# Optimization experiments

Hardware: AMD Instinct MI355X
Metric: run time of the kernel (lower is better)

Reference implementation:

```python
import jax, jax.numpy as jnp
import numpy as np

D_MODEL = 1024
N_HEADS = 16
HEAD_DIM = D_MODEL // N_HEADS
RSQRT = 1.0 / np.sqrt(HEAD_DIM).astype(np.float32)


def setup_inputs() -> dict:
    key = jax.random.key(0)
    k1, k2, k3 = jax.random.split(key, 3)
    bs, sl = 4, 2048
    x = jax.random.normal(k1, (bs, sl, D_MODEL), dtype=jnp.float32)
    # stored as (in, out) so forward is x @ w; same math as torch Linear (no bias)
    w_qkv = jax.random.normal(k2, (D_MODEL, 3 * D_MODEL), dtype=jnp.float32) * 0.02
    w_proj = jax.random.normal(k3, (D_MODEL, D_MODEL), dtype=jnp.float32) * 0.02
    return {"x": x, "w_qkv": w_qkv, "w_proj": w_proj}


def reference(x, w_qkv, w_proj):
    bs, sl, dm = x.shape
    qkv = x @ w_qkv                                   # (bs, sl, 3*dm)
    q, k, v = jnp.split(qkv, 3, axis=-1)
    # (bs, sl, n, hd) -> (bs, n, sl, hd)
    q = q.reshape(bs, sl, N_HEADS, HEAD_DIM).transpose(0, 2, 1, 3)
    k = k.reshape(bs, sl, N_HEADS, HEAD_DIM).transpose(0, 2, 1, 3)
    v = v.reshape(bs, sl, N_HEADS, HEAD_DIM).transpose(0, 2, 1, 3)
    attn = jnp.einsum("bnqd,bnkd->bnqk", q, k) * RSQRT  # (bs, n, sl, sl)
    causal = jnp.tril(jnp.ones((sl, sl), dtype=bool))
    attn = jnp.where(causal[None, None], attn, -jnp.inf)
    attn = jax.nn.softmax(attn, axis=-1)
    out = jnp.einsum("bnqk,bnkd->bnqd", attn, v)      # (bs, n, sl, hd)
    out = out.transpose(0, 2, 1, 3).reshape(bs, sl, dm)
    return out @ w_proj
```

## Files before the change

kernel.cpp:

```cpp
#include <hip/hip_runtime.h>
#include <stdint.h>
#include <math.h>

typedef __attribute__((ext_vector_type(8))) short short8;
typedef __attribute__((ext_vector_type(4))) float f32x4;
typedef __attribute__((ext_vector_type(16))) float f32x16;

#define DEV __device__ __forceinline__

DEV unsigned short f2bf(float f) {
  union { float f; unsigned int u; } v; v.f = f;
  return (unsigned short)((v.u + 0x7FFFu + ((v.u >> 16) & 1u)) >> 16);
}

DEV unsigned int pkbf(float a, float b) {
  unsigned int r;
  asm("v_cvt_pk_bf16_f32 %0, %1, %2" : "=v"(r) : "v"(a), "v"(b));
  return r;
}

#if __has_builtin(__builtin_amdgcn_permlane32_swap)
DEV float redsum32(float v) {
  typedef __attribute__((ext_vector_type(2))) unsigned int uint2v;
  union { float f; unsigned int u; } c; c.f = v;
  uint2v r = __builtin_amdgcn_permlane32_swap(c.u, c.u, false, false);
  union { unsigned int u; float f; } a, b; a.u = r[0]; b.u = r[1];
  return a.f + b.f;
}
#else
DEV float redsum32(float v) { return v + __shfl_xor(v, 32, 64); }
#endif

DEV void gld16(const void* g, void* lds) {
  __builtin_amdgcn_global_load_lds(
      (const __attribute__((address_space(1))) unsigned int*)g,
      (__attribute__((address_space(3))) unsigned int*)lds, 16, 0, 0);
}

__global__ __launch_bounds__(256) void cvt_bf16_kernel(
    const float* __restrict__ in, unsigned short* __restrict__ out, int n) {
  int i = (blockIdx.x * 256 + threadIdx.x) * 8;
  if (i >= n) return;
  const float4 a = *(const float4*)(in + i);
  const float4 b = *(const float4*)(in + i + 4);
  short8 o;
  o[0] = (short)f2bf(a.x); o[1] = (short)f2bf(a.y);
  o[2] = (short)f2bf(a.z); o[3] = (short)f2bf(a.w);
  o[4] = (short)f2bf(b.x); o[5] = (short)f2bf(b.y);
  o[6] = (short)f2bf(b.z); o[7] = (short)f2bf(b.w);
  *(short8*)(out + i) = o;
}

__global__ __launch_bounds__(256) void transpose_w_kernel(
    const float* __restrict__ in, unsigned short* __restrict__ out,
    int Kdim, int Ndim) {
  __shared__ float t[32][33];
  const int nb = blockIdx.x * 32, kb = blockIdx.y * 32;
  const int tx = threadIdx.x & 31, ty = threadIdx.x >> 5;
#pragma unroll
  for (int i = 0; i < 32; i += 8)
    t[ty + i][tx] = in[(size_t)(kb + ty + i) * Ndim + nb + tx];
  __syncthreads();
#pragma unroll
  for (int i = 0; i < 32; i += 8)
    out[(size_t)(nb + ty + i) * Kdim + kb + tx] = f2bf(t[tx][ty + i]);
}

template<int M, int N, int K, int MODE>
__global__ __launch_bounds__(256)
void gemm_bt_kernel(const unsigned short* __restrict__ A,
                    const unsigned short* __restrict__ Bt,
                    unsigned short* __restrict__ Qd,
                    unsigned short* __restrict__ Kd,
                    unsigned short* __restrict__ Vd,
                    float* __restrict__ outC) {
  __shared__ __align__(16) unsigned short lsA[128 * 32];
  __shared__ __align__(16) unsigned short lsB[128 * 32];
  const int tid = threadIdx.x, wid = tid >> 6, lane = tid & 63;
  const int wr = wid >> 1, wc = wid & 1;
  constexpr int nx = N / 128;
  constexpr int nwg = (M / 128) * nx;
  static_assert(nwg % 8 == 0, "bijective XCD swizzle needs nwg % 8 == 0");
  int id = blockIdx.y * nx + blockIdx.x;
  id = (id & 7) * (nwg / 8) + (id >> 3);
  const int m0 = (id / nx) * 128, n0 = (id % nx) * 128;

  f32x4 acc[4][4] = {};

  const int rA = lane >> 2, kA = (lane & 3) * 8;
  for (int kt = 0; kt < K / 32; ++kt) {
    __syncthreads();
#pragma unroll
    for (int c = 0; c < 2; ++c) {
      const int q = c * 4 + wid;
      gld16(A  + (size_t)(m0 + q * 16 + rA) * K + kt * 32 + kA, lsA + q * 512);
      gld16(Bt + (size_t)(n0 + q * 16 + rA) * K + kt * 32 + kA, lsB + q * 512);
    }
    __syncthreads();
    short8 af[4], bfr[4];
#pragma unroll
    for (int i = 0; i < 4; ++i) {
      af[i]  = *(const short8*)(lsA + (wr * 64 + i * 16 + (lane & 15)) * 32 + (lane >> 4) * 8);
      bfr[i] = *(const short8*)(lsB + (wc * 64 + i * 16 + (lane & 15)) * 32 + (lane >> 4) * 8);
    }
#pragma unroll
    for (int i = 0; i < 4; ++i)
#pragma unroll
      for (int j = 0; j < 4; ++j)
        acc[i][j] = __builtin_amdgcn_mfma_f32_16x16x32_bf16(af[i], bfr[j], acc[i][j], 0, 0, 0);
  }

#pragma unroll
  for (int i = 0; i < 4; ++i) {
#pragma unroll
    for (int j = 0; j < 4; ++j) {
      const int rbase = m0 + wr * 64 + i * 16 + (lane >> 4) * 4;
      const int col = n0 + wc * 64 + j * 16 + (lane & 15);
      if constexpr (MODE == 0) {
        const int which = col >> 10, hh = (col >> 6) & 15, d = col & 63;
        unsigned short* dst = which == 0 ? Qd : (which == 1 ? Kd : Vd);
        const float scale = which == 0 ? 0.18033688f : 1.0f;
        const int sd = d >> 4, hi = (d >> 3) & 1, jd = d & 7;
        const int t2 = d >> 5, qlv = d & 31;
#pragma unroll
        for (int ii = 0; ii < 4; ++ii) {
          const int r = rbase + ii, b = r >> 11, seq = r & 2047;
          size_t idx;
          if (which == 2) {
            const int kt2 = seq >> 5, sl = (seq >> 4) & 1, g = seq & 15;
            const int u = (g & 3) | ((g & 4) << 1) | ((g & 8) >> 1);
            idx = ((((size_t)(b * 16 + hh) * 64 + kt2) * 4 + (t2 * 2 + sl)) * 64
                   + qlv + 32 * (u >> 3)) * 8 + (u & 7);
          } else {
            idx = ((((size_t)(b * 16 + hh) * 64 + (seq >> 5)) * 4 + sd) * 64
                   + (seq & 31) + 32 * hi) * 8 + jd;
          }
          dst[idx] = f2bf(acc[i][j][ii] * scale);
        }
      } else {
#pragma unroll
        for (int ii = 0; ii < 4; ++ii)
          outC[(size_t)(rbase + ii) * N + col] = acc[i][j][ii];
      }
    }
  }
}

DEV void loadK4f(const unsigned short* Kfb, int kt, int lane, short8 kf[4]) {
  const unsigned short* p = Kfb + (size_t)kt * 2048 + lane * 8;
#pragma unroll
  for (int s = 0; s < 4; ++s) kf[s] = *(const short8*)(p + s * 512);
}
DEV void loadV4f(const unsigned short* Vfb, int kt, int lane, short8 vf[4]) {
  const unsigned short* p = Vfb + (size_t)kt * 2048 + lane * 8;
#pragma unroll
  for (int f = 0; f < 4; ++f) vf[f] = *(const short8*)(p + f * 512);
}

template<int NP, bool MASK>
DEV void attn_step(int kv0, const short8 kf[4], const short8 qf[][4],
                   const int q0[], const short8 vf[4],
                   float l[], f32x16 o[][2], int ql, int h) {
  f32x16 st[NP];
  __builtin_amdgcn_s_setprio(1);
#pragma unroll
  for (int pp = 0; pp < NP; ++pp) {
    f32x16 s = {};
#pragma unroll
    for (int ss = 0; ss < 4; ++ss)
      s = __builtin_amdgcn_mfma_f32_32x32x16_bf16(kf[ss], qf[pp][ss], s, 0, 0, 0);
    st[pp] = s;
  }
  __builtin_amdgcn_s_setprio(0);
  if constexpr (MASK) {
#pragma unroll
    for (int r = 0; r < 16; ++r) {
      const int krow = (r & 3) + 8 * (r >> 2) + 4 * h;
      if (kv0 + krow > q0[0] + ql) st[0][r] = -INFINITY;
    }
  }
  union pk_t { unsigned int u[4]; short8 s8; };
  pk_t f0[NP], f1[NP];
#pragma unroll
  for (int pp = 0; pp < NP; ++pp) {
    float p[16];
#pragma unroll
    for (int r = 0; r < 16; ++r) p[r] = exp2f(fminf(st[pp][r], 64.f));
    float ps = ((p[0] + p[1]) + (p[2] + p[3])) + ((p[4] + p[5]) + (p[6] + p[7]));
    ps += ((p[8] + p[9]) + (p[10] + p[11])) + ((p[12] + p[13]) + (p[14] + p[15]));
    l[pp] += ps;
#pragma unroll
    for (int i = 0; i < 4; ++i) {
      f0[pp].u[i] = pkbf(p[2 * i], p[2 * i + 1]);
      f1[pp].u[i] = pkbf(p[8 + 2 * i], p[9 + 2 * i]);
    }
  }
  __builtin_amdgcn_s_setprio(1);
#pragma unroll
  for (int pp = 0; pp < NP; ++pp) {
    o[pp][0] = __builtin_amdgcn_mfma_f32_32x32x16_bf16(vf[0], f0[pp].s8, o[pp][0], 0, 0, 0);
    o[pp][0] = __builtin_amdgcn_mfma_f32_32x32x16_bf16(vf[1], f1[pp].s8, o[pp][0], 0, 0, 0);
    o[pp][1] = __builtin_amdgcn_mfma_f32_32x32x16_bf16(vf[2], f0[pp].s8, o[pp][1], 0, 0, 0);
    o[pp][1] = __builtin_amdgcn_mfma_f32_32x32x16_bf16(vf[3], f1[pp].s8, o[pp][1], 0, 0, 0);
  }
  __builtin_amdgcn_s_setprio(0);
}

__global__ __launch_bounds__(256, 2)
void attn_kernel(const unsigned short* __restrict__ Qf,
                 const unsigned short* __restrict__ Kf,
                 const unsigned short* __restrict__ Vf,
                 unsigned short* __restrict__ O) {
  const int bh = blockIdx.x & 63;
  const int w  = blockIdx.x >> 6;
  const int wid = threadIdx.x >> 6, lane = threadIdx.x & 63;
  const int ql = lane & 31, h = lane >> 5;
  const int qtA = w * 4 + wid;
  const int qtB = 63 - qtA;
  const int q0[2] = {qtA * 32, qtB * 32};

  const unsigned short* Qfb = Qf + (size_t)bh * 131072;
  const unsigned short* Kfb = Kf + (size_t)bh * 131072;
  const unsigned short* Vfb = Vf + (size_t)bh * 131072;

  short8 qf[2][4];
#pragma unroll
  for (int pp = 0; pp < 2; ++pp) {
    const int qt = pp == 0 ? qtA : qtB;
#pragma unroll
    for (int s = 0; s < 4; ++s)
      qf[pp][s] = *(const short8*)(Qfb + (size_t)qt * 2048 + s * 512 + lane * 8);
  }

  f32x16 o[2][2] = {};
  float l[2] = {0.f, 0.f};

  short8 kf[4], kn[4], vf[4];
  loadK4f(Kfb, 0, lane, kf);

  for (int t = 0; t < qtA; ++t) {
    loadV4f(Vfb, t, lane, vf);
    loadK4f(Kfb, t + 1, lane, kn);
    attn_step<2, false>(0, kf, qf, q0, vf, l, o, ql, h);
#pragma unroll
    for (int s = 0; s < 4; ++s) kf[s] = kn[s];
  }
  {
    loadV4f(Vfb, qtA, lane, vf);
    loadK4f(Kfb, qtA + 1, lane, kn);
    attn_step<2, true>(qtA * 32, kf, qf, q0, vf, l, o, ql, h);
#pragma unroll
    for (int s = 0; s < 4; ++s) kf[s] = kn[s];
  }
  for (int t = qtA + 1; t < qtB; ++t) {
    loadV4f(Vfb, t, lane, vf);
    loadK4f(Kfb, t + 1, lane, kn);
    attn_step<1, false>(0, kf, &qf[1], &q0[1], vf, &l[1], &o[1], ql, h);
#pragma unroll
    for (int s = 0; s < 4; ++s) kf[s] = kn[s];
  }
  {
    loadV4f(Vfb, qtB, lane, vf);
    attn_step<1, true>(qtB * 32, kf, &qf[1], &q0[1], vf, &l[1], &o[1], ql, h);
  }

  const int b = bh >> 4, head = bh & 15;
#pragma unroll
  for (int pp = 0; pp < 2; ++pp) {
    const float inv = 1.0f / redsum32(l[pp]);
    unsigned short* Orow = O + ((size_t)(b * 2048 + q0[pp] + ql)) * 1024 + head * 64;
#pragma unroll
    for (int g = 0; g < 4; ++g) {
      {
        const unsigned int lo = pkbf(o[pp][0][g * 4 + 0] * inv, o[pp][0][g * 4 + 1] * inv);
        const unsigned int hi = pkbf(o[pp][0][g * 4 + 2] * inv, o[pp][0][g * 4 + 3] * inv);
        uint2 val; val.x = lo; val.y = hi;
        *(uint2*)(Orow + 8 * g + 4 * h) = val;
      }
      {
        const unsigned int lo = pkbf(o[pp][1][g * 4 + 0] * inv, o[pp][1][g * 4 + 1] * inv);
        const unsigned int hi = pkbf(o[pp][1][g * 4 + 2] * inv, o[pp][1][g * 4 + 3] * inv);
        uint2 val; val.x = lo; val.y = hi;
        *(uint2*)(Orow + 32 + 8 * g + 4 * h) = val;
      }
    }
  }
}

extern "C" void kernel_launch(void* const* d_in, const int* in_sizes, int n_in,
                              void* d_out, int out_size, void* d_ws, size_t ws_size,
                              hipStream_t stream) {
  (void)in_sizes; (void)n_in; (void)out_size; (void)ws_size;
  const float* x      = (const float*)d_in[0];
  const float* w_qkv  = (const float*)d_in[1];
  const float* w_proj = (const float*)d_in[2];
  float* out = (float*)d_out;
  char* ws = (char*)d_ws;

  unsigned short* x_bf   = (unsigned short*)(ws);
  unsigned short* wqT    = (unsigned short*)(ws + 16777216);
  unsigned short* wpT    = (unsigned short*)(ws + 23068672);
  unsigned short* Qfd    = (unsigned short*)(ws + 25165824);
  unsigned short* Kfd    = (unsigned short*)(ws + 41943040);
  unsigned short* Vfd    = (unsigned short*)(ws + 58720256);
  unsigned short* attn_o = x_bf;

  cvt_bf16_kernel<<<4096, 256, 0, stream>>>(x, x_bf, 8388608);
  transpose_w_kernel<<<dim3(96, 32), 256, 0, stream>>>(w_qkv, wqT, 1024, 3072);
  transpose_w_kernel<<<dim3(32, 32), 256, 0, stream>>>(w_proj, wpT, 1024, 1024);
  gemm_bt_kernel<8192, 3072, 1024, 0><<<dim3(24, 64), 256, 0, stream>>>(
      x_bf, wqT, Qfd, Kfd, Vfd, nullptr);
  attn_kernel<<<512, 256, 0, stream>>>(Qfd, Kfd, Vfd, attn_o);
  gemm_bt_kernel<8192, 1024, 1024, 1><<<dim3(8, 64), 256, 0, stream>>>(
      attn_o, wpT, nullptr, nullptr, nullptr, out);
}
```

Before: 183.5 us.

## Split attention KV range across two waves per query tile and combine via LDS

Doubles the attention block to 512 threads so each query-tile pair is handled by two waves that take alternating (even/odd) key tiles, then merges their partial outputs and row sums through shared memory before normalizing and writing. The aim is more wave-level parallelism and latency hiding in the attention kernel, which had only 4 waves per block with long serial KV loops. The merge relies on softmax without running-max rescaling, so the two partials can simply be added. In exchange it adds an LDS combine, a block barrier, and a larger LDS footprint, and the prefetch stride of two tiles may weaken cache reuse.

```diff
diff --git a/kernel.cpp b/kernel.cpp
--- a/kernel.cpp
+++ b/kernel.cpp
@@ -206,18 +206,28 @@
   __builtin_amdgcn_s_setprio(0);
 }
 
-__global__ __launch_bounds__(256, 2)
+__global__ __launch_bounds__(512)
 void attn_kernel(const unsigned short* __restrict__ Qf,
                  const unsigned short* __restrict__ Kf,
                  const unsigned short* __restrict__ Vf,
                  unsigned short* __restrict__ O) {
+  __shared__ __align__(16) f32x4 cmb[4][16][64];
+  __shared__ float cml[4][2][64];
   const int bh = blockIdx.x & 63;
   const int w  = blockIdx.x >> 6;
   const int wid = threadIdx.x >> 6, lane = threadIdx.x & 63;
+  const int widp = wid & 3, piv = wid >> 2;
   const int ql = lane & 31, h = lane >> 5;
-  const int qtA = w * 4 + wid;
+  const int qtA = w * 4 + widp;
   const int qtB = 63 - qtA;
   const int q0[2] = {qtA * 32, qtB * 32};
+
+  const int L = qtA - ((qtA - piv) & 1);
+  const bool ownA = ((qtA & 1) == piv);
+  const int stopU = ownA ? qtA - 2 : L;
+  const int sB = L + 2;
+  const bool ownB = !ownA;
+  const int stopB = ownB ? qtB - 2 : qtB - 1;
 
   const unsigned short* Qfb = Qf + (size_t)bh * 131072;
   const unsigned short* Kfb = Kf + (size_t)bh * 131072;
@@ -236,52 +246,80 @@
   float l[2] = {0.f, 0.f};
 
   short8 kf[4], kn[4], vf[4];
-  loadK4f(Kfb, 0, lane, kf);
-
-  for (int t = 0; t < qtA; ++t) {
+  loadK4f(Kfb, piv, lane, kf);
+
+  for (int t = piv; t <= stopU; t += 2) {
     loadV4f(Vfb, t, lane, vf);
-    loadK4f(Kfb, t + 1, lane, kn);
+    loadK4f(Kfb, t + 2, lane, kn);
     attn_step<2, false>(0, kf, qf, q0, vf, l, o, ql, h);
 #pragma unroll
     for (int s = 0; s < 4; ++s) kf[s] = kn[s];
   }
-  {
+  if (ownA) {
     loadV4f(Vfb, qtA, lane, vf);
-    loadK4f(Kfb, qtA + 1, lane, kn);
+    loadK4f(Kfb, qtA + 2, lane, kn);
     attn_step<2, true>(qtA * 32, kf, qf, q0, vf, l, o, ql, h);
 #pragma unroll
     for (int s = 0; s < 4; ++s) kf[s] = kn[s];
   }
-  for (int t = qtA + 1; t < qtB; ++t) {
+  for (int t = sB; t <= stopB; t += 2) {
     loadV4f(Vfb, t, lane, vf);
-    loadK4f(Kfb, t + 1, lane, kn);
+    int tp = t + 2; if (tp > 63) tp = 63;
+    loadK4f(Kfb, tp, lane, kn);
     attn_step<1, false>(0, kf, &qf[1], &q0[1], vf, &l[1], &o[1], ql, h);
 #pragma unroll
     for (int s = 0; s < 4; ++s) kf[s] = kn[s];
   }
-  {
+  if (ownB) {
     loadV4f(Vfb, qtB, lane, vf);
     attn_step<1, true>(qtB * 32, kf, &qf[1], &q0[1], vf, &l[1], &o[1], ql, h);
   }
 
-  const int b = bh >> 4, head = bh & 15;
-#pragma unroll
-  for (int pp = 0; pp < 2; ++pp) {
-    const float inv = 1.0f / redsum32(l[pp]);
-    unsigned short* Orow = O + ((size_t)(b * 2048 + q0[pp] + ql)) * 1024 + head * 64;
-#pragma unroll
-    for (int g = 0; g < 4; ++g) {
-      {
-        const unsigned int lo = pkbf(o[pp][0][g * 4 + 0] * inv, o[pp][0][g * 4 + 1] * inv);
-        const unsigned int hi = pkbf(o[pp][0][g * 4 + 2] * inv, o[pp][0][g * 4 + 3] * inv);
-        uint2 val; val.x = lo; val.y = hi;
-        *(uint2*)(Orow + 8 * g + 4 * h) = val;
-      }
-      {
-        const unsigned int lo = pkbf(o[pp][1][g * 4 + 0] * inv, o[pp][1][g * 4 + 1] * inv);
-        const unsigned int hi = pkbf(o[pp][1][g * 4 + 2] * inv, o[pp][1][g * 4 + 3] * inv);
-        uint2 val; val.x = lo; val.y = hi;
-        *(uint2*)(Orow + 32 + 8 * g + 4 * h) = val;
+  if (piv) {
+#pragma unroll
+    for (int pp = 0; pp < 2; ++pp) {
+      cml[widp][pp][lane] = l[pp];
+#pragma unroll
+      for (int hd = 0; hd < 2; ++hd)
+#pragma unroll
+        for (int g = 0; g < 4; ++g) {
+          f32x4 v;
+          v[0] = o[pp][hd][4 * g + 0]; v[1] = o[pp][hd][4 * g + 1];
+          v[2] = o[pp][hd][4 * g + 2]; v[3] = o[pp][hd][4 * g + 3];
+          cmb[widp][pp * 8 + hd * 4 + g][lane] = v;
+        }
+    }
+  }
+  __syncthreads();
+  if (!piv) {
+    const int b = bh >> 4, head = bh & 15;
+#pragma unroll
+    for (int pp = 0; pp < 2; ++pp) {
+      l[pp] += cml[widp][pp][lane];
+#pragma unroll
+      for (int hd = 0; hd < 2; ++hd)
+#pragma unroll
+        for (int g = 0; g < 4; ++g) {
+          const f32x4 v = cmb[widp][pp * 8 + hd * 4 + g][lane];
+          o[pp][hd][4 * g + 0] += v[0]; o[pp][hd][4 * g + 1] += v[1];
+          o[pp][hd][4 * g + 2] += v[2]; o[pp][hd][4 * g + 3] += v[3];
+        }
+      const float inv = 1.0f / redsum32(l[pp]);
+      unsigned short* Orow = O + ((size_t)(b * 2048 + q0[pp] + ql)) * 1024 + head * 64;
+#pragma unroll
+      for (int g = 0; g < 4; ++g) {
+        {
+          const unsigned int lo = pkbf(o[pp][0][g * 4 + 0] * inv, o[pp][0][g * 4 + 1] * inv);
+          const unsigned int hi = pkbf(o[pp][0][g * 4 + 2] * inv, o[pp][0][g * 4 + 3] * inv);
+          uint2 val; val.x = lo; val.y = hi;
+          *(uint2*)(Orow + 8 * g + 4 * h) = val;
+        }
+        {
+          const unsigned int lo = pkbf(o[pp][1][g * 4 + 0] * inv, o[pp][1][g * 4 + 1] * inv);
+          const unsigned int hi = pkbf(o[pp][1][g * 4 + 2] * inv, o[pp][1][g * 4 + 3] * inv);
+          uint2 val; val.x = lo; val.y = hi;
+          *(uint2*)(Orow + 32 + 8 * g + 4 * h) = val;
+        }
       }
     }
   }
@@ -310,7 +348,7 @@
   transpose_w_kernel<<<dim3(32, 32), 256, 0, stream>>>(w_proj, wpT, 1024, 1024);
   gemm_bt_kernel<8192, 3072, 1024, 0><<<dim3(24, 64), 256, 0, stream>>>(
       x_bf, wqT, Qfd, Kfd, Vfd, nullptr);
-  attn_kernel<<<512, 256, 0, stream>>>(Qfd, Kfd, Vfd, attn_o);
+  attn_kernel<<<512, 512, 0, stream>>>(Qfd, Kfd, Vfd, attn_o);
   gemm_bt_kernel<8192, 1024, 1024, 1><<<dim3(8, 64), 256, 0, stream>>>(
       attn_o, wpT, nullptr, nullptr, nullptr, out);
 }
```

Result: no change. 185.2 us (+0.9%).
